# Kernel tuning notes

Measured on AMD Instinct MI355X. Metric: run time of the kernel, lower is better.

Reference implementation:

```python
import jax, jax.numpy as jnp
import numpy as np


def log_g(x):
    # log of g(x) = where(x>=0, x+0.5, sigmoid(x)), computed stably in log space
    return jnp.where(x >= 0, jnp.log(jax.nn.relu(x) + 0.5), -jax.nn.softplus(-x))


def setup_inputs() -> dict:
    key = jax.random.key(0)
    k1, k2, k3, k4 = jax.random.split(key, 4)
    B, S, D, Di = 4, 8192, 512, 1024
    X = jax.random.normal(k1, (B, S, D), dtype=jnp.float32)
    # prev_hidden must be strictly positive (its log is taken)
    hidden = jax.random.uniform(k2, (B, 1, Di), dtype=jnp.float32) * 0.9 + 0.1
    W_hg = jax.random.normal(k3, (2 * Di, D), dtype=jnp.float32) * 0.02
    W_out = jax.random.normal(k4, (D, Di), dtype=jnp.float32) * 0.02
    return {"X": X, "hidden": hidden, "W_hg": W_hg, "W_out": W_out}


def reference(X, hidden, W_hg, W_out):
    # X: [B,S,D]; hidden: [B,1,Di]; W_hg: [2Di,D]; W_out: [D,Di]
    S = X.shape[1]
    hg = jnp.einsum('bsd,ed->bse', X, W_hg)            # [B,S,2Di]
    h, gate = jnp.split(hg, 2, axis=-1)                # each [B,S,Di]

    log_coeffs = -jax.nn.softplus(gate)                # log(1 - z)
    log_z = -jax.nn.softplus(-gate)                    # log z
    log_values = log_z + log_g(h)                      # log(z * g(h_tilde))

    # prepend prev hidden state
    log_values = jnp.concatenate([jnp.log(hidden), log_values], axis=1)  # [B,S+1,Di]
    log_coeffs = jnp.pad(log_coeffs, ((0, 0), (1, 0), (0, 0)))           # [B,S+1,Di]

    # Heinsen associative scan in log space
    a_star = jnp.cumsum(log_coeffs, axis=1)
    log_h = a_star + jax.lax.cumlogsumexp(log_values - a_star, axis=1)
    h_all = jnp.exp(log_h)[:, -S:]                     # [B,S,Di]

    next_prev_hidden = h_all[:, -1:]                   # [B,1,Di]
    out = jnp.einsum('bsi,di->bsd', h_all, W_out)      # [B,S,D]
    return out, next_prev_hidden
```

## Files before the change

### kernel.cpp

```cpp
#include <hip/hip_runtime.h>
#include <hip/hip_bf16.h>
#include <stdint.h>

typedef __attribute__((ext_vector_type(8))) short short8;
typedef __attribute__((ext_vector_type(4))) float f32x4;

#define CH 64
#define NC 128

__device__ __forceinline__ unsigned short f2bf(float f) {
  union { float f; unsigned u; } x; x.f = f;
  unsigned u = x.u;
  u = (u + 0x7fffu + ((u >> 16) & 1u)) >> 16;
  return (unsigned short)u;
}
__device__ __forceinline__ float bf2f(unsigned u16) {
  union { unsigned u; float f; } x; x.u = u16 << 16;
  return x.f;
}

#define GLOAD_LDS16(gptr, lptr) \
  __builtin_amdgcn_global_load_lds((const __attribute__((address_space(1))) void*)(gptr), \
                                   (__attribute__((address_space(3))) void*)(lptr), 16, 0, 0)

#define NQ_X   4194304
#define NQ_WHG  262144
#define NQ_WOUT 131072
__global__ void k_cvt_all(const float* __restrict__ X, const float* __restrict__ Whg,
                          const float* __restrict__ Wout,
                          unsigned short* __restrict__ Xb, unsigned short* __restrict__ Whgb,
                          unsigned short* __restrict__ Woutb) {
  int i = blockIdx.x * blockDim.x + threadIdx.x;
  const float* src; unsigned short* dst; int off;
  if (i < NQ_X)                { src = X;    dst = Xb;    off = i; }
  else if (i < NQ_X + NQ_WHG)  { src = Whg;  dst = Whgb;  off = i - NQ_X; }
  else                         { src = Wout; dst = Woutb; off = i - NQ_X - NQ_WHG; }
  float4 f = reinterpret_cast<const float4*>(src)[off];
  ushort4 o = make_ushort4(f2bf(f.x), f2bf(f.y), f2bf(f.z), f2bf(f.w));
  reinterpret_cast<ushort4*>(dst)[off] = o;
}

__global__ __launch_bounds__(256, 2) void k_gemm1(
    const unsigned short* __restrict__ Xb,
    const unsigned short* __restrict__ Wb,
    uint32_t* __restrict__ avArr,
    float* __restrict__ Acar, float* __restrict__ Vcar)
{
  __shared__ unsigned short As[128 * 64];
  __shared__ unsigned short Bs0[128 * 64];
  __shared__ unsigned short Bs1[128 * 64];

  const int bid  = blockIdx.x;
  const int xcd  = bid & 7;
  const int loc  = bid >> 3;
  const int at   = loc >> 3;
  const int yt   = loc & 7;
  const int m0 = (xcd * 32 + at) * 128;
  const int i0 = yt * 128;
  const int tid = threadIdx.x;
  const int lane = tid & 63;
  const int wave = tid >> 6;
  const int wm = (wave >> 1) * 64;
  const int wn = (wave & 1) * 64;
  const int srow = tid >> 3;
  const int scol = (tid & 7) * 8;

  f32x4 acc0[4][4], acc1[4][4];
#pragma unroll
  for (int f = 0; f < 4; ++f)
#pragma unroll
    for (int g = 0; g < 4; ++g) {
      acc0[f][g] = f32x4{0.f, 0.f, 0.f, 0.f};
      acc1[f][g] = f32x4{0.f, 0.f, 0.f, 0.f};
    }

  for (int k0 = 0; k0 < 512; k0 += 64) {
    __syncthreads();
#pragma unroll
    for (int j = 0; j < 4; ++j) {
      int row = j * 32 + srow;
      GLOAD_LDS16(Xb + (size_t)(m0 + row) * 512 + k0 + scol, As + row * 64 + scol);
    }
#pragma unroll
    for (int j = 0; j < 4; ++j) {
      int row = j * 32 + srow;
      GLOAD_LDS16(Wb + (size_t)(i0 + row) * 512 + k0 + scol, Bs0 + row * 64 + scol);
    }
#pragma unroll
    for (int j = 0; j < 4; ++j) {
      int row = j * 32 + srow;
      GLOAD_LDS16(Wb + (size_t)(1024 + i0 + row) * 512 + k0 + scol, Bs1 + row * 64 + scol);
    }
    __syncthreads();

#pragma unroll
    for (int kk = 0; kk < 2; ++kk) {
      const int kof = kk * 32 + (lane >> 4) * 8;
      const int rl = lane & 15;
      short8 av[4], b0[4], b1[4];
#pragma unroll
      for (int f = 0; f < 4; ++f)
        av[f] = *(const short8*)(As + (wm + f * 16 + rl) * 64 + kof);
#pragma unroll
      for (int g = 0; g < 4; ++g) {
        b0[g] = *(const short8*)(Bs0 + (wn + g * 16 + rl) * 64 + kof);
        b1[g] = *(const short8*)(Bs1 + (wn + g * 16 + rl) * 64 + kof);
      }
#pragma unroll
      for (int f = 0; f < 4; ++f)
#pragma unroll
        for (int g = 0; g < 4; ++g) {
          acc0[f][g] = __builtin_amdgcn_mfma_f32_16x16x32_bf16(av[f], b0[g], acc0[f][g], 0, 0, 0);
          acc1[f][g] = __builtin_amdgcn_mfma_f32_16x16x32_bf16(av[f], b1[g], acc1[f][g], 0, 0, 0);
        }
    }
  }

  const int rl = lane & 15;
  const int q  = lane >> 4;
  const int mb = m0 + wm;
  const int b  = mb >> 13;
  const int c  = (mb & 8191) >> 6;

#pragma unroll
  for (int g = 0; g < 4; ++g) {
    const int i = i0 + wn + g * 16 + rl;
    float Achunk = 1.f, Vchunk = 0.f;
#pragma unroll
    for (int f = 0; f < 4; ++f) {
      float Aseg = 1.f, Vseg = 0.f;
#pragma unroll
      for (int r = 0; r < 4; ++r) {
        float h    = acc0[f][g][r];
        float gate = acc1[f][g][r];
        float e  = __expf(gate);
        float ac = __builtin_amdgcn_rcpf(1.f + e);
        float z  = e * ac;
        float gg;
        if (h >= 0.f) gg = h + 0.5f;
        else { float eh = __expf(h); gg = eh * __builtin_amdgcn_rcpf(1.f + eh); }
        float v = z * gg;
        int m = mb + f * 16 + q * 4 + r;
        avArr[(size_t)m * 1024 + i] = (uint32_t)f2bf(ac) | ((uint32_t)f2bf(v) << 16);
        Vseg = Vseg * ac + v;
        Aseg = Aseg * ac;
      }
      {
        float Ap = __shfl_xor(Aseg, 16);
        float Vp = __shfl_xor(Vseg, 16);
        if (q & 1) { Vseg = Vp * Aseg + Vseg; Aseg = Ap * Aseg; }
        else       { Vseg = Vseg * Ap + Vp;   Aseg = Aseg * Ap; }
      }
      {
        float Ap = __shfl_xor(Aseg, 32);
        float Vp = __shfl_xor(Vseg, 32);
        if (q & 2) { Vseg = Vp * Aseg + Vseg; Aseg = Ap * Aseg; }
        else       { Vseg = Vseg * Ap + Vp;   Aseg = Aseg * Ap; }
      }
      Vchunk = Vchunk * Aseg + Vseg;
      Achunk = Achunk * Aseg;
    }
    if (lane < 16) {
      size_t co = ((size_t)b * NC + c) * 1024 + i;
      Acar[co] = Achunk;
      Vcar[co] = Vchunk;
    }
  }
}

__global__ void k_scanB(const float* __restrict__ hidden,
                        const float* __restrict__ Acar, const float* __restrict__ Vcar,
                        float* __restrict__ Hstart)
{
  int t = blockIdx.x * blockDim.x + threadIdx.x;
  int b = t >> 10, i = t & 1023;
  float H = hidden[(size_t)b * 1024 + i];
  for (int c = 0; c < NC; ++c) {
    size_t o = ((size_t)b * NC + c) * 1024 + i;
    Hstart[o] = H;
    H = fmaf(Acar[o], H, Vcar[o]);
  }
}

__global__ void k_scanC(const uint32_t* __restrict__ av,
                        const float* __restrict__ Hstart,
                        unsigned short* __restrict__ hAll, float* __restrict__ nextH)
{
  int c = blockIdx.x & (NC - 1);
  int b = blockIdx.x >> 7;
  size_t base4 = (((size_t)b * 8192 + (size_t)c * CH) * 1024) / 4 + threadIdx.x;
  size_t ho = (((size_t)b * NC + c) * 1024) / 4 + threadIdx.x;
  float4 H = reinterpret_cast<const float4*>(Hstart)[ho];
#pragma unroll 4
  for (int t = 0; t < CH; ++t) {
    uint4 u = reinterpret_cast<const uint4*>(av)[base4 + (size_t)t * 256];
    H.x = fmaf(bf2f(u.x & 0xffffu), H.x, bf2f(u.x >> 16));
    H.y = fmaf(bf2f(u.y & 0xffffu), H.y, bf2f(u.y >> 16));
    H.z = fmaf(bf2f(u.z & 0xffffu), H.z, bf2f(u.z >> 16));
    H.w = fmaf(bf2f(u.w & 0xffffu), H.w, bf2f(u.w >> 16));
    ushort4 o = make_ushort4(f2bf(H.x), f2bf(H.y), f2bf(H.z), f2bf(H.w));
    reinterpret_cast<ushort4*>(hAll)[base4 + (size_t)t * 256] = o;
  }
  if (c == NC - 1)
    reinterpret_cast<float4*>(nextH)[(size_t)b * 256 + threadIdx.x] = H;
}

__global__ __launch_bounds__(256, 2) void k_gemm2(
    const unsigned short* __restrict__ Ab,
    const unsigned short* __restrict__ Bb,
    float* __restrict__ out)
{
  __shared__ unsigned short As[128 * 64];
  __shared__ unsigned short Bs[128 * 64];

  const int m0 = blockIdx.y * 128;
  const int n0 = blockIdx.x * 128;
  const int tid = threadIdx.x;
  const int lane = tid & 63;
  const int wave = tid >> 6;
  const int wm = (wave >> 1) * 64;
  const int wn = (wave & 1) * 64;
  const int srow = tid >> 3;
  const int scol = (tid & 7) * 8;

  f32x4 acc[4][4];
#pragma unroll
  for (int f = 0; f < 4; ++f)
#pragma unroll
    for (int g = 0; g < 4; ++g) acc[f][g] = f32x4{0.f, 0.f, 0.f, 0.f};

  for (int k0 = 0; k0 < 1024; k0 += 64) {
    __syncthreads();
#pragma unroll
    for (int j = 0; j < 4; ++j) {
      int row = j * 32 + srow;
      GLOAD_LDS16(Ab + (size_t)(m0 + row) * 1024 + k0 + scol, As + row * 64 + scol);
    }
#pragma unroll
    for (int j = 0; j < 4; ++j) {
      int row = j * 32 + srow;
      GLOAD_LDS16(Bb + (size_t)(n0 + row) * 1024 + k0 + scol, Bs + row * 64 + scol);
    }
    __syncthreads();

#pragma unroll
    for (int kk = 0; kk < 2; ++kk) {
      const int kof = kk * 32 + (lane >> 4) * 8;
      const int rl = lane & 15;
      short8 av[4], bv[4];
#pragma unroll
      for (int f = 0; f < 4; ++f)
        av[f] = *(const short8*)(As + (wm + f * 16 + rl) * 64 + kof);
#pragma unroll
      for (int g = 0; g < 4; ++g)
        bv[g] = *(const short8*)(Bs + (wn + g * 16 + rl) * 64 + kof);
#pragma unroll
      for (int f = 0; f < 4; ++f)
#pragma unroll
        for (int g = 0; g < 4; ++g)
          acc[f][g] = __builtin_amdgcn_mfma_f32_16x16x32_bf16(av[f], bv[g], acc[f][g], 0, 0, 0);
    }
  }

  const int rl = lane & 15;
  const int rr = (lane >> 4) * 4;
#pragma unroll
  for (int f = 0; f < 4; ++f)
#pragma unroll
    for (int g = 0; g < 4; ++g)
#pragma unroll
      for (int r = 0; r < 4; ++r) {
        int m = m0 + wm + f * 16 + rr + r;
        int n = n0 + wn + g * 16 + rl;
        out[(size_t)m * 512 + n] = acc[f][g][r];
      }
}

extern "C" void kernel_launch(void* const* d_in, const int* in_sizes, int n_in,
                              void* d_out, int out_size, void* d_ws, size_t ws_size,
                              hipStream_t stream) {
  const float* X      = (const float*)d_in[0];
  const float* hidden = (const float*)d_in[1];
  const float* W_hg   = (const float*)d_in[2];
  const float* W_out  = (const float*)d_in[3];

  float* out   = (float*)d_out;
  float* nextH = out + (size_t)32768 * 512;

  char* ws = (char*)d_ws;
  size_t off = 0;
  auto alloc = [&](size_t bytes) -> void* {
    void* p = ws + off;
    off = (off + bytes + 255) & ~(size_t)255;
    return p;
  };
  unsigned short* Xb    = (unsigned short*)alloc(32768ULL * 512 * 2);
  unsigned short* Whgb  = (unsigned short*)alloc(2048ULL * 512 * 2);
  unsigned short* Woutb = (unsigned short*)alloc(512ULL * 1024 * 2);
  unsigned short* hAll  = (unsigned short*)alloc(32768ULL * 1024 * 2);
  float*    Acar   = (float*)alloc(4ULL * NC * 1024 * 4);
  float*    Vcar   = (float*)alloc(4ULL * NC * 1024 * 4);
  float*    Hstart = (float*)alloc(4ULL * NC * 1024 * 4);
  uint32_t* avArr  = (uint32_t*)alloc(32768ULL * 1024 * 4);

  k_cvt_all<<<17920, 256, 0, stream>>>(X, W_hg, W_out, Xb, Whgb, Woutb);

  k_gemm1<<<2048, 256, 0, stream>>>(Xb, Whgb, avArr, Acar, Vcar);

  k_scanB<<<16, 256, 0, stream>>>(hidden, Acar, Vcar, Hstart);
  k_scanC<<<512, 256, 0, stream>>>(avArr, Hstart, hAll, nextH);

  dim3 g2(4, 256);
  k_gemm2<<<g2, 256, 0, stream>>>(hAll, Woutb, out);
}
```

Measured before the change: 316.2 us.

## Triple-buffer GEMM1 LDS tiles with async global-to-LDS prefetch

Restructures the first GEMM's K loop from synchronous 64-wide K steps into 16 steps of 32-wide K tiles held in a three-slot LDS ring buffer. Loads for tile t+2 are issued before computing tile t, and waits use vmcnt counters plus a single barrier per step, so global load latency is meant to overlap with MFMA work. LDS use rises from 48KB to 72KB per block, which may limit occupancy at two blocks per CU. The 32-element rows can also change LDS bank-conflict behavior.

```diff
diff --git a/kernel.cpp b/kernel.cpp
--- a/kernel.cpp
+++ b/kernel.cpp
@@ -40,15 +40,14 @@
   reinterpret_cast<ushort4*>(dst)[off] = o;
 }
 
+#define TILE_ELEMS 12288
 __global__ __launch_bounds__(256, 2) void k_gemm1(
     const unsigned short* __restrict__ Xb,
     const unsigned short* __restrict__ Wb,
     uint32_t* __restrict__ avArr,
     float* __restrict__ Acar, float* __restrict__ Vcar)
 {
-  __shared__ unsigned short As[128 * 64];
-  __shared__ unsigned short Bs0[128 * 64];
-  __shared__ unsigned short Bs1[128 * 64];
+  __shared__ unsigned short lds[3 * TILE_ELEMS];
 
   const int bid  = blockIdx.x;
   const int xcd  = bid & 7;
@@ -62,8 +61,25 @@
   const int wave = tid >> 6;
   const int wm = (wave >> 1) * 64;
   const int wn = (wave & 1) * 64;
-  const int srow = tid >> 3;
-  const int scol = (tid & 7) * 8;
+
+  const int srow2 = tid >> 2;
+  const int sc8   = (tid & 3) * 8;
+
+  const unsigned short* gA  = Xb + (size_t)(m0 + srow2) * 512 + sc8;
+  const unsigned short* gB0 = Wb + (size_t)(i0 + srow2) * 512 + sc8;
+  const unsigned short* gB1 = Wb + (size_t)(1024 + i0 + srow2) * 512 + sc8;
+  unsigned short* lA  = lds + srow2 * 32 + sc8;
+  unsigned short* lB0 = lA + 4096;
+  unsigned short* lB1 = lA + 8192;
+
+#define STAGE(bi, t) do { \
+    GLOAD_LDS16(gA  + (t) * 32,         lA  + (bi) * TILE_ELEMS); \
+    GLOAD_LDS16(gA  + (t) * 32 + 32768, lA  + (bi) * TILE_ELEMS + 2048); \
+    GLOAD_LDS16(gB0 + (t) * 32,         lB0 + (bi) * TILE_ELEMS); \
+    GLOAD_LDS16(gB0 + (t) * 32 + 32768, lB0 + (bi) * TILE_ELEMS + 2048); \
+    GLOAD_LDS16(gB1 + (t) * 32,         lB1 + (bi) * TILE_ELEMS); \
+    GLOAD_LDS16(gB1 + (t) * 32 + 32768, lB1 + (bi) * TILE_ELEMS + 2048); \
+  } while (0)
 
   f32x4 acc0[4][4], acc1[4][4];
 #pragma unroll
@@ -74,49 +90,48 @@
       acc1[f][g] = f32x4{0.f, 0.f, 0.f, 0.f};
     }
 
-  for (int k0 = 0; k0 < 512; k0 += 64) {
-    __syncthreads();
-#pragma unroll
-    for (int j = 0; j < 4; ++j) {
-      int row = j * 32 + srow;
-      GLOAD_LDS16(Xb + (size_t)(m0 + row) * 512 + k0 + scol, As + row * 64 + scol);
-    }
-#pragma unroll
-    for (int j = 0; j < 4; ++j) {
-      int row = j * 32 + srow;
-      GLOAD_LDS16(Wb + (size_t)(i0 + row) * 512 + k0 + scol, Bs0 + row * 64 + scol);
-    }
-#pragma unroll
-    for (int j = 0; j < 4; ++j) {
-      int row = j * 32 + srow;
-      GLOAD_LDS16(Wb + (size_t)(1024 + i0 + row) * 512 + k0 + scol, Bs1 + row * 64 + scol);
-    }
-    __syncthreads();
-
-#pragma unroll
-    for (int kk = 0; kk < 2; ++kk) {
-      const int kof = kk * 32 + (lane >> 4) * 8;
-      const int rl = lane & 15;
-      short8 av[4], b0[4], b1[4];
-#pragma unroll
-      for (int f = 0; f < 4; ++f)
-        av[f] = *(const short8*)(As + (wm + f * 16 + rl) * 64 + kof);
+  const int rl = lane & 15;
+  const int q8 = (lane >> 4) * 8;
+  const int aoff = (wm + rl) * 32 + q8;
+  const int boff = (wn + rl) * 32 + q8;
+
+  STAGE(0, 0);
+  STAGE(1, 1);
+  asm volatile("s_waitcnt vmcnt(6)" ::: "memory");
+  __builtin_amdgcn_s_barrier();
+  __builtin_amdgcn_sched_barrier(0);
+
+#pragma unroll
+  for (int t = 0; t < 16; ++t) {
+    if (t + 2 < 16) STAGE((t + 2) % 3, t + 2);
+
+    const unsigned short* bb = lds + (t % 3) * TILE_ELEMS;
+    short8 av[4], b0[4], b1[4];
+#pragma unroll
+    for (int f = 0; f < 4; ++f)
+      av[f] = *(const short8*)(bb + aoff + f * 512);
+#pragma unroll
+    for (int g = 0; g < 4; ++g) {
+      b0[g] = *(const short8*)(bb + 4096 + boff + g * 512);
+      b1[g] = *(const short8*)(bb + 8192 + boff + g * 512);
+    }
+#pragma unroll
+    for (int f = 0; f < 4; ++f)
 #pragma unroll
       for (int g = 0; g < 4; ++g) {
-        b0[g] = *(const short8*)(Bs0 + (wn + g * 16 + rl) * 64 + kof);
-        b1[g] = *(const short8*)(Bs1 + (wn + g * 16 + rl) * 64 + kof);
-      }
-#pragma unroll
-      for (int f = 0; f < 4; ++f)
-#pragma unroll
-        for (int g = 0; g < 4; ++g) {
-          acc0[f][g] = __builtin_amdgcn_mfma_f32_16x16x32_bf16(av[f], b0[g], acc0[f][g], 0, 0, 0);
-          acc1[f][g] = __builtin_amdgcn_mfma_f32_16x16x32_bf16(av[f], b1[g], acc1[f][g], 0, 0, 0);
-        }
-    }
-  }
-
-  const int rl = lane & 15;
+        acc0[f][g] = __builtin_amdgcn_mfma_f32_16x16x32_bf16(av[f], b0[g], acc0[f][g], 0, 0, 0);
+        acc1[f][g] = __builtin_amdgcn_mfma_f32_16x16x32_bf16(av[f], b1[g], acc1[f][g], 0, 0, 0);
+      }
+
+    if (t < 15) {
+      if (t + 2 < 16) { asm volatile("s_waitcnt vmcnt(6)" ::: "memory"); }
+      else            { asm volatile("s_waitcnt vmcnt(0)" ::: "memory"); }
+      __builtin_amdgcn_s_barrier();
+      __builtin_amdgcn_sched_barrier(0);
+    }
+  }
+#undef STAGE
+
   const int q  = lane >> 4;
   const int mb = m0 + wm;
   const int b  = mb >> 13;
```

Result: faster. 302.9 us (-4.2%).
